# Kernel optimization log

Measured on AMD Instinct MI355X. Metric: run time of the kernel, lower is better.

## Reference

```python
import jax, jax.numpy as jnp
import numpy as np

N = 24000; E = 384000; NT = 3; IN = 128; HID = 32; ED = 64; NE = 5; FFN = 64; C = 16
HEADS = (8, 8, 1); ALPHA = 0.05; DAL = 2


def _lrelu(x, s):
    return jnp.where(x >= 0, x, s * x)


def _elu(x):
    return jnp.where(x > 0, x, jnp.expm1(x))


def _ln(x, g, b, eps=1e-5):
    m = x.mean(-1, keepdims=True)
    v = ((x - m) ** 2).mean(-1, keepdims=True)
    return (x - m) / jnp.sqrt(v + eps) * g + b


def _l2n(x, eps=1e-12):
    return x / jnp.maximum(jnp.linalg.norm(x, axis=1, keepdims=True), eps)


def _ta(h, src, dst, e_feat, edge_emb, W, We, al, ar, ae, bias, res_W, res_attn, act):
    # SimpleHGN-style heterogeneous graph attention layer (TALayer)
    Hh = al.shape[0]
    feat = (h @ W).reshape(N, Hh, HID)                       # [N,H,D]
    ee = (edge_emb[e_feat] @ We).reshape(E, Hh, ED)          # [E,H,ED]
    el = (feat * al).sum(-1)                                 # [N,H]
    er = (feat * ar).sum(-1)                                 # [N,H]
    lg = _lrelu(el[src] + er[dst] + (ee * ae).sum(-1), 0.2)  # [E,H]
    m = jax.ops.segment_max(lg, dst, num_segments=N)         # edge softmax over dst
    a = jnp.exp(lg - m[dst])
    a = a / jax.ops.segment_sum(a, dst, num_segments=N)[dst]
    if res_attn is not None:
        a = a * (1.0 - ALPHA) + res_attn * ALPHA             # residual attention carry-over
    rst = jax.ops.segment_sum(a[:, :, None] * feat[src], dst, num_segments=N)
    if res_W is not None:
        rst = rst + (h @ res_W).reshape(N, Hh, HID)
    rst = rst + bias
    if act:
        rst = _elu(rst)
    return rst, jax.lax.stop_gradient(a)


def forward(feats, fc_W, fc_b, ntype_emb, W_ntype,
            ta0_edge_emb, ta0_W, ta0_We, ta0_al, ta0_ar, ta0_ae, ta0_bias,
            ta1_edge_emb, ta1_W, ta1_We, ta1_al, ta1_ar, ta1_ae, ta1_bias, ta1_res_W,
            ta2_edge_emb, ta2_W, ta2_We, ta2_al, ta2_ar, ta2_ae, ta2_bias, ta2_res_W,
            da_ln1_g, da_ln1_b, da_Wq, da_bq, da_Wk, da_bk, da_Wv, da_bv, da_Wo, da_bo,
            da_ln2_g, da_ln2_b, da_W1, da_b1, da_W2, da_b2, final_W, logits_W,
            e_feat, node_type, src, dst):
    # per-node-type input projection + leaky_relu(0.01), concat over types -> [N,HID]
    h = _lrelu(jnp.einsum('tni,tio->tno', feats, fc_W) + fc_b[:, None, :], 0.01).reshape(N, HID)
    ntype_feat = (ntype_emb @ W_ntype)[node_type]            # [N,HID]
    h = h * ntype_feat
    h0, a0 = _ta(h, src, dst, e_feat, ta0_edge_emb, ta0_W, ta0_We, ta0_al, ta0_ar, ta0_ae, ta0_bias, None, None, True)
    h = h0.reshape(N, -1)
    h1, _ = _ta(h, src, dst, e_feat, ta1_edge_emb, ta1_W, ta1_We, ta1_al, ta1_ar, ta1_ae, ta1_bias, ta1_res_W, a0, True)
    h = h1.reshape(N, -1)
    hf, _ = _ta(h, src, dst, e_feat, ta2_edge_emb, ta2_W, ta2_We, ta2_al, ta2_ar, ta2_ae, ta2_bias, ta2_res_W, None, False)
    h_feat = hf.reshape(N, HID)
    # dim-wise transformer (DALayer stack): tokens = HID dims, channel = 1
    x = (h_feat * ntype_feat)[:, :, None]                    # [N,HID,1]
    for l in range(DAL):
        y = _ln(x, da_ln1_g[l], da_ln1_b[l])
        q = y @ da_Wq[l] + da_bq[l]
        k = y @ da_Wk[l] + da_bk[l]
        v = y @ da_Wv[l] + da_bv[l]
        att = jax.nn.softmax(jnp.einsum('nqd,nkd->nqk', q, k), axis=-1)  # scale=att_size**-0.5=1
        x = x + (jnp.einsum('nqk,nkd->nqd', att, v) @ da_Wo[l] + da_bo[l])
        y = _ln(x, da_ln2_g[l], da_ln2_b[l])
        x = x + (jax.nn.gelu(y @ da_W1[l] + da_b1[l], approximate=False) @ da_W2[l] + da_b2[l])
    h_dim = _l2n(x[:, :, 0])
    h_final = jnp.concatenate([_l2n(h_feat), h_dim], axis=1) @ final_W
    logits = jax.nn.relu(h_final) @ logits_W
    return logits / jnp.maximum(jnp.linalg.norm(logits, axis=1, keepdims=True), 1e-12)


def setup_inputs():
    key = jax.random.key(0)
    ks = iter(jax.random.split(key, 96))
    def rn(shape, s=0.1):
        return jax.random.normal(next(ks), shape, jnp.float32) * s
    inp = {}
    inp["feats"] = jax.random.normal(next(ks), (NT, N // NT, IN), jnp.float32)
    inp["e_feat"] = jax.random.randint(next(ks), (E,), 0, NE)
    inp["node_type"] = jax.random.randint(next(ks), (N,), 0, NT)
    inp["src"] = jax.random.randint(next(ks), (E,), 0, N)
    inp["dst"] = jax.random.randint(next(ks), (E,), 0, N)
    inp["fc_W"] = rn((NT, IN, HID)); inp["fc_b"] = rn((NT, HID))
    inp["ntype_emb"] = rn((NT, HID)); inp["W_ntype"] = rn((HID, HID))
    ins = (HID, HID * HEADS[0], HID * HEADS[1])
    for l in range(3):
        Hh = HEADS[l]; di = ins[l]; p = "ta%d_" % l
        inp[p + "edge_emb"] = rn((NE, ED))
        inp[p + "W"] = rn((di, Hh * HID))
        inp[p + "We"] = rn((ED, Hh * ED))
        inp[p + "al"] = rn((Hh, HID)); inp[p + "ar"] = rn((Hh, HID)); inp[p + "ae"] = rn((Hh, ED))
        inp[p + "bias"] = jnp.zeros((Hh, HID), jnp.float32)
        if l > 0:
            inp[p + "res_W"] = rn((di, Hh * HID))
    inp["da_ln1_g"] = jnp.ones((DAL, 1), jnp.float32); inp["da_ln1_b"] = jnp.zeros((DAL, 1), jnp.float32)
    inp["da_Wq"] = rn((DAL, 1, 1)); inp["da_bq"] = jnp.zeros((DAL, 1), jnp.float32)
    inp["da_Wk"] = rn((DAL, 1, 1)); inp["da_bk"] = jnp.zeros((DAL, 1), jnp.float32)
    inp["da_Wv"] = rn((DAL, 1, 1)); inp["da_bv"] = jnp.zeros((DAL, 1), jnp.float32)
    inp["da_Wo"] = rn((DAL, 1, 1)); inp["da_bo"] = jnp.zeros((DAL, 1), jnp.float32)
    inp["da_ln2_g"] = jnp.ones((DAL, 1), jnp.float32); inp["da_ln2_b"] = jnp.zeros((DAL, 1), jnp.float32)
    inp["da_W1"] = rn((DAL, 1, FFN)); inp["da_b1"] = jnp.zeros((DAL, FFN), jnp.float32)
    inp["da_W2"] = rn((DAL, FFN, 1)); inp["da_b2"] = jnp.zeros((DAL, 1), jnp.float32)
    inp["final_W"] = rn((2 * HID, HID))
    inp["logits_W"] = rn((HID, C))
    return inp


def reference(feats, fc_W, fc_b, ntype_emb, W_ntype,
              ta0_edge_emb, ta0_W, ta0_We, ta0_al, ta0_ar, ta0_ae, ta0_bias,
              ta1_edge_emb, ta1_W, ta1_We, ta1_al, ta1_ar, ta1_ae, ta1_bias, ta1_res_W,
              ta2_edge_emb, ta2_W, ta2_We, ta2_al, ta2_ar, ta2_ae, ta2_bias, ta2_res_W,
              da_ln1_g, da_ln1_b, da_Wq, da_bq, da_Wk, da_bk, da_Wv, da_bv, da_Wo, da_bo,
              da_ln2_g, da_ln2_b, da_W1, da_b1, da_W2, da_b2, final_W, logits_W,
              e_feat, node_type, src, dst):
    return forward(feats, fc_W, fc_b, ntype_emb, W_ntype,
                   ta0_edge_emb, ta0_W, ta0_We, ta0_al, ta0_ar, ta0_ae, ta0_bias,
                   ta1_edge_emb, ta1_W, ta1_We, ta1_al, ta1_ar, ta1_ae, ta1_bias, ta1_res_W,
                   ta2_edge_emb, ta2_W, ta2_We, ta2_al, ta2_ar, ta2_ae, ta2_bias, ta2_res_W,
                   da_ln1_g, da_ln1_b, da_Wq, da_bq, da_Wk, da_bk, da_Wv, da_bv, da_Wo, da_bo,
                   da_ln2_g, da_ln2_b, da_W1, da_b1, da_W2, da_b2, final_W, logits_W,
                   e_feat, node_type, src, dst)
```

## Files before the change

kernel.cpp:

```cpp
#include <hip/hip_runtime.h>
#include <math.h>

constexpr int kN = 24000;
constexpr int kE = 384000;
constexpr float kAlpha = 0.05f;

typedef unsigned int   u32;
typedef unsigned short u16;
typedef __attribute__((ext_vector_type(8))) short short8;
typedef __attribute__((ext_vector_type(4))) float float4v;

__device__ __forceinline__ float bf2f(u16 x) { return __uint_as_float(((u32)x) << 16); }
__device__ __forceinline__ u16 f2bf(float f) {
  u32 u = __float_as_uint(f);
  return (u16)((u + 0x7fffu + ((u >> 16) & 1u)) >> 16);
}

__global__ void __launch_bounds__(256) zero_ints_kernel(int* __restrict__ p, int n) {
  int i = blockIdx.x * 256 + threadIdx.x;
  if (i < n) p[i] = 0;
}

__global__ void __launch_bounds__(256) count_kernel(const int* __restrict__ dst,
                                                    int* __restrict__ counts) {
  int e = blockIdx.x * 256 + threadIdx.x;
  if (e < kE) atomicAdd(&counts[dst[e]], 1);
}

__global__ void __launch_bounds__(1024) scan_kernel(const int* __restrict__ counts,
                                                    int* __restrict__ row_start) {
  __shared__ int wsum[16];
  __shared__ int carry_s;
  int tid = threadIdx.x, lane = tid & 63, wid = tid >> 6;
  if (tid == 0) { carry_s = 0; row_start[0] = 0; }
  __syncthreads();
  for (int base = 0; base < kN; base += 1024) {
    int x = (base + tid < kN) ? counts[base + tid] : 0;
    #pragma unroll
    for (int off = 1; off < 64; off <<= 1) {
      int y = __shfl_up(x, off);
      if (lane >= off) x += y;
    }
    if (lane == 63) wsum[wid] = x;
    __syncthreads();
    if (tid < 16) {
      int wv = wsum[tid];
      #pragma unroll
      for (int off = 1; off < 16; off <<= 1) {
        int y = __shfl_up(wv, off);
        if (tid >= off) wv += y;
      }
      wsum[tid] = wv;
    }
    __syncthreads();
    int incl = x + carry_s + (wid > 0 ? wsum[wid - 1] : 0);
    if (base + tid < kN) row_start[base + tid + 1] = incl;
    __syncthreads();
    if (tid == 1023) carry_s = incl;
    __syncthreads();
  }
}

__global__ void __launch_bounds__(256) scatter_kernel(const int* __restrict__ dst,
                                                      const int* __restrict__ row_start,
                                                      int* __restrict__ cursor,
                                                      int* __restrict__ edge_ids) {
  int e = blockIdx.x * 256 + threadIdx.x;
  if (e < kE) {
    int n = dst[e];
    int pos = row_start[n] + atomicAdd(&cursor[n], 1);
    edge_ids[pos] = e;
  }
}

__global__ void __launch_bounds__(256) prepack_kernel(
    const float* __restrict__ W0, const float* __restrict__ al0, const float* __restrict__ ar0,
    const float* __restrict__ W1, const float* __restrict__ al1, const float* __restrict__ ar1,
    const float* __restrict__ rW1,
    const float* __restrict__ W2, const float* __restrict__ al2, const float* __restrict__ ar2,
    const float* __restrict__ rW2,
    u16* __restrict__ WT0, u16* __restrict__ WT1, u16* __restrict__ WT2,
    const float* __restrict__ ntype_emb, const float* __restrict__ W_ntype,
    const float* __restrict__ emb0, const float* __restrict__ We0, const float* __restrict__ ae0,
    const float* __restrict__ emb1, const float* __restrict__ We1, const float* __restrict__ ae1,
    const float* __restrict__ emb2, const float* __restrict__ We2, const float* __restrict__ ae2,
    const float* __restrict__ ln1_b, const float* __restrict__ Wv, const float* __restrict__ bv,
    const float* __restrict__ Wo, const float* __restrict__ bo,
    const float* __restrict__ ln2_b, const float* __restrict__ DW1, const float* __restrict__ Db1,
    const float* __restrict__ DW2, const float* __restrict__ Db2,
    float* __restrict__ ntf, float* __restrict__ eterm, float* __restrict__ dadelta) {
  __shared__ float wae[17][64];
  __shared__ float red[128];
  int tid = threadIdx.x;
  if (blockIdx.x < 744) {
    const int SZ0 = 320 * 32, SZ1 = 576 * 256;
    int gid = blockIdx.x * 256 + tid;
    float v = 0.f;
    if (gid < SZ0) {
      int n = gid / 32, k = gid % 32;
      if (n < 256) v = W0[k * 256 + n];
      else if (n < 264) { int h = n - 256; for (int d = 0; d < 32; ++d) v += W0[k * 256 + h * 32 + d] * al0[h * 32 + d]; }
      else if (n < 272) { int h = n - 264; for (int d = 0; d < 32; ++d) v += W0[k * 256 + h * 32 + d] * ar0[h * 32 + d]; }
      WT0[n * 32 + k] = f2bf(v);
    } else if (gid < SZ0 + SZ1) {
      int i = gid - SZ0;
      int n = i / 256, k = i % 256;
      if (n < 256) v = W1[k * 256 + n];
      else if (n < 264) { int h = n - 256; for (int d = 0; d < 32; ++d) v += W1[k * 256 + h * 32 + d] * al1[h * 32 + d]; }
      else if (n < 272) { int h = n - 264; for (int d = 0; d < 32; ++d) v += W1[k * 256 + h * 32 + d] * ar1[h * 32 + d]; }
      else if (n < 528) v = rW1[k * 256 + (n - 272)];
      WT1[n * 256 + k] = f2bf(v);
    } else {
      int i = gid - SZ0 - SZ1;
      int n = i / 256, k = i % 256;
      if (n < 32) v = W2[k * 32 + n];
      else if (n == 32) { for (int d = 0; d < 32; ++d) v += W2[k * 32 + d] * al2[d]; }
      else if (n == 33) { for (int d = 0; d < 32; ++d) v += W2[k * 32 + d] * ar2[d]; }
      else if (n < 66) v = rW2[k * 32 + (n - 34)];
      WT2[n * 256 + k] = f2bf(v);
    }
  } else {
    for (int idx = tid; idx < 17 * 64; idx += 256) {
      int hg = idx >> 6, k = idx & 63;
      const float* We; const float* ae; int Hh, h;
      if (hg < 8)       { We = We0; ae = ae0; Hh = 8; h = hg; }
      else if (hg < 16) { We = We1; ae = ae1; Hh = 8; h = hg - 8; }
      else              { We = We2; ae = ae2; Hh = 1; h = 0; }
      float s = 0.f;
      for (int d = 0; d < 64; ++d) s += We[(size_t)k * Hh * 64 + h * 64 + d] * ae[h * 64 + d];
      wae[hg][k] = s;
    }
    __syncthreads();
    for (int id = tid; id < 85; id += 256) {
      const float* emb; int Hh, t, h, hg, base;
      if (id < 40)      { emb = emb0; Hh = 8; t = id / 8;  h = id % 8; hg = h;      base = 0;  }
      else if (id < 80) { int i = id - 40; emb = emb1; Hh = 8; t = i / 8; h = i % 8; hg = 8 + h; base = 40; }
      else              { int i = id - 80; emb = emb2; Hh = 1; t = i;    h = 0;     hg = 16;    base = 80; }
      float s = 0.f;
      for (int k = 0; k < 64; ++k) s += emb[t * 64 + k] * wae[hg][k];
      eterm[base + t * Hh + h] = s;
    }
    for (int idx = tid; idx < 96; idx += 256) {
      int t = idx / 32, o = idx % 32;
      float s = 0.f;
      for (int k = 0; k < 32; ++k) s += ntype_emb[t * 32 + k] * W_ntype[k * 32 + o];
      ntf[idx] = s;
    }
    for (int i2 = tid; i2 < 128; i2 += 256) {
      int l = i2 >> 6, j = i2 & 63;
      float u = ln2_b[l] * DW1[l * 64 + j] + Db1[l * 64 + j];
      float g = 0.5f * u * (1.0f + erff(u * 0.7071067811865476f));
      red[i2] = g * DW2[l * 64 + j];
    }
    __syncthreads();
    if (tid == 0) {
      float delta = 0.f;
      for (int l = 0; l < 2; ++l) {
        float vs = ln1_b[l] * Wv[l] + bv[l];
        delta += vs * Wo[l] + bo[l] + Db2[l];
      }
      for (int i = 0; i < 128; ++i) delta += red[i];
      *dadelta = delta;
    }
  }
}

__global__ void __launch_bounds__(256) inproj_kernel(
    const float* __restrict__ feats, const float* __restrict__ fc_W,
    const float* __restrict__ fc_b, const float* __restrict__ ntf,
    const int* __restrict__ node_type, u16* __restrict__ hb) {
  int t = blockIdx.x * 256 + threadIdx.x;
  if (t >= kN * 32) return;
  int n = t >> 5, o = t & 31;
  int ty = n / 8000;
  const float* fr = &feats[(size_t)n * 128];
  const float* w  = &fc_W[(size_t)ty * 4096 + o];
  float s = fc_b[ty * 32 + o];
  #pragma unroll
  for (int k = 0; k < 128; k += 4) {
    float4 f = *(const float4*)&fr[k];
    s += f.x * w[(k + 0) * 32] + f.y * w[(k + 1) * 32]
       + f.z * w[(k + 2) * 32] + f.w * w[(k + 3) * 32];
  }
  s = (s < 0.f) ? 0.01f * s : s;
  hb[t] = f2bf(s * ntf[node_type[n] * 32 + o]);
}

template <int K>
__global__ void __launch_bounds__(256) mfma_gemm_kernel(
    const u16* __restrict__ A, const u16* __restrict__ WT,
    const float* __restrict__ bias,
    u16* __restrict__ featb, float* __restrict__ el, float* __restrict__ er,
    u16* __restrict__ resb, float* __restrict__ resf,
    int N1, int HH, int N2) {
  constexpr int RB = K * 2;
  constexpr int CPR = K / 8;
  __shared__ __align__(16) u16 As[64 * K];
  __shared__ __align__(16) u16 Bs[64 * K];
  const int tid = threadIdx.x;
  const int l = tid & 63;
  const int w = tid >> 6;
  const int wm = w >> 1, wn = w & 1;
  const int m0 = blockIdx.y * 64;
  const int n0 = blockIdx.x * 64;
  const int kslot = l >> 4;
  const int l15 = l & 15;

  #pragma unroll
  for (int c = tid; c < 64 * CPR; c += 256) {
    int row = c / CPR, ch = c - row * CPR;
    int off = (row * RB + ch * 16) ^ ((row & 7) << 4);
    uint4 va = *(const uint4*)(A + (size_t)(m0 + row) * K + ch * 8);
    *(uint4*)((char*)As + off) = va;
    uint4 vb = *(const uint4*)(WT + (size_t)(n0 + row) * K + ch * 8);
    *(uint4*)((char*)Bs + off) = vb;
  }
  __syncthreads();

  float4v acc[2][2];
  #pragma unroll
  for (int f = 0; f < 2; ++f)
    #pragma unroll
    for (int g = 0; g < 2; ++g) { acc[f][g][0]=0.f; acc[f][g][1]=0.f; acc[f][g][2]=0.f; acc[f][g][3]=0.f; }

  #pragma unroll
  for (int kc = 0; kc < K; kc += 32) {
    short8 af[2], bf[2];
    #pragma unroll
    for (int f = 0; f < 2; ++f) {
      int row = wm * 32 + f * 16 + l15;
      int off = (row * RB + kc * 2 + kslot * 16) ^ ((row & 7) << 4);
      af[f] = *(const short8*)((const char*)As + off);
    }
    #pragma unroll
    for (int g = 0; g < 2; ++g) {
      int n = wn * 32 + g * 16 + l15;
      int off = (n * RB + kc * 2 + kslot * 16) ^ ((n & 7) << 4);
      bf[g] = *(const short8*)((const char*)Bs + off);
    }
    #pragma unroll
    for (int f = 0; f < 2; ++f)
      #pragma unroll
      for (int g = 0; g < 2; ++g)
        acc[f][g] = __builtin_amdgcn_mfma_f32_16x16x32_bf16(af[f], bf[g], acc[f][g], 0, 0, 0);
  }

  const int rbase = kslot * 4;
  #pragma unroll
  for (int f = 0; f < 2; ++f) {
    #pragma unroll
    for (int g = 0; g < 2; ++g) {
      int gc = n0 + wn * 32 + g * 16 + l15;
      #pragma unroll
      for (int reg = 0; reg < 4; ++reg) {
        int gr = m0 + wm * 32 + f * 16 + rbase + reg;
        float v = acc[f][g][reg];
        if (gc < N1) {
          featb[(size_t)gr * N1 + gc] = f2bf(v);
        } else if (gc < N1 + HH) {
          el[(size_t)gr * HH + (gc - N1)] = v;
        } else if (gc < N1 + 2 * HH) {
          er[(size_t)gr * HH + (gc - N1 - HH)] = v;
        } else if (gc < N1 + 2 * HH + N2) {
          int c2 = gc - N1 - 2 * HH;
          float vv = v + bias[c2];
          if (resb) resb[(size_t)gr * N2 + c2] = f2bf(vv);
          else      resf[(size_t)gr * N2 + c2] = vv;
        }
      }
    }
  }
}

template <bool WRITE_A0, bool READ_A0, bool BIAS_INIT, bool ACT>
__global__ void __launch_bounds__(256) agg8w_kernel(
    const int* __restrict__ row_start, const int* __restrict__ edge_ids,
    const int* __restrict__ src, const int* __restrict__ ef,
    const float* __restrict__ el, const float* __restrict__ er,
    const float* __restrict__ eterm,
    const u16* __restrict__ featb,
    const float* __restrict__ bias,
    _Float16* __restrict__ a0h,
    const u16* __restrict__ accb,
    u16* __restrict__ outb) {
  int n = (blockIdx.x * 256 + threadIdx.x) >> 6;
  if (n >= kN) return;
  int l = threadIdx.x & 63;
  int h = l >> 3, s = l & 7;
  int s0 = row_start[n], s1 = row_start[n + 1];
  float ern = er[n * 8 + h];
  float et0 = eterm[0 * 8 + h], et1 = eterm[1 * 8 + h], et2 = eterm[2 * 8 + h];
  float et3 = eterm[3 * 8 + h], et4 = eterm[4 * 8 + h];
  float m = -1e30f, ssum = 0.f;
  for (int i = s0 + s; i < s1; i += 8) {
    int e = edge_ids[i];
    int efc = ef[e];
    float etv = (efc == 0) ? et0 : (efc == 1) ? et1 : (efc == 2) ? et2 : (efc == 3) ? et3 : et4;
    float lg = el[src[e] * 8 + h] + ern + etv;
    lg = (lg < 0.f) ? 0.2f * lg : lg;
    if (lg > m) { ssum = ssum * expf(m - lg) + 1.f; m = lg; }
    else        { ssum += expf(lg - m); }
  }
  #pragma unroll
  for (int mk = 1; mk <= 4; mk <<= 1) {
    float om = __shfl_xor(m, mk);
    float os = __shfl_xor(ssum, mk);
    float nm = fmaxf(m, om);
    ssum = ssum * expf(m - nm) + os * expf(om - nm);
    m = nm;
  }
  float inv = 1.f / ssum;
  const size_t rowoff = (size_t)n * 256 + h * 32 + s * 4;
  float4 acc;
  if (BIAS_INIT) {
    acc = *(const float4*)(bias + h * 32 + s * 4);
  } else {
    ushort4 rv = *(const ushort4*)(accb + rowoff);
    acc = make_float4(bf2f(rv.x), bf2f(rv.y), bf2f(rv.z), bf2f(rv.w));
  }
  int i = s0;
  for (; i + 8 <= s1; i += 8) {
    int e = edge_ids[i + s];
    int sek = src[e];
    int efc = ef[e];
    float etv = (efc == 0) ? et0 : (efc == 1) ? et1 : (efc == 2) ? et2 : (efc == 3) ? et3 : et4;
    float lg = el[sek * 8 + h] + ern + etv;
    lg = (lg < 0.f) ? 0.2f * lg : lg;
    float am = expf(lg - m) * inv;
    if (WRITE_A0) a0h[(size_t)e * 8 + h] = (_Float16)am;
    if (READ_A0)  am = am * (1.f - kAlpha) + (float)a0h[(size_t)e * 8 + h] * kAlpha;
    #pragma unroll
    for (int j = 0; j < 8; ++j) {
      float aj = __shfl(am, (h << 3) + j);
      int sej = __shfl(sek, j);
      ushort4 fv = *(const ushort4*)(featb + (size_t)sej * 256 + h * 32 + s * 4);
      acc.x = fmaf(aj, bf2f(fv.x), acc.x);
      acc.y = fmaf(aj, bf2f(fv.y), acc.y);
      acc.z = fmaf(aj, bf2f(fv.z), acc.z);
      acc.w = fmaf(aj, bf2f(fv.w), acc.w);
    }
  }
  if (i < s1) {
    int cnt = s1 - i;
    float am = 0.f; int sek = 0;
    if (s < cnt) {
      int e = edge_ids[i + s];
      sek = src[e];
      int efc = ef[e];
      float etv = (efc == 0) ? et0 : (efc == 1) ? et1 : (efc == 2) ? et2 : (efc == 3) ? et3 : et4;
      float lg = el[sek * 8 + h] + ern + etv;
      lg = (lg < 0.f) ? 0.2f * lg : lg;
      am = expf(lg - m) * inv;
      if (WRITE_A0) a0h[(size_t)e * 8 + h] = (_Float16)am;
      if (READ_A0)  am = am * (1.f - kAlpha) + (float)a0h[(size_t)e * 8 + h] * kAlpha;
    }
    for (int j = 0; j < cnt; ++j) {
      float aj = __shfl(am, (h << 3) + j);
      int sej = __shfl(sek, j);
      ushort4 fv = *(const ushort4*)(featb + (size_t)sej * 256 + h * 32 + s * 4);
      acc.x = fmaf(aj, bf2f(fv.x), acc.x);
      acc.y = fmaf(aj, bf2f(fv.y), acc.y);
      acc.z = fmaf(aj, bf2f(fv.z), acc.z);
      acc.w = fmaf(aj, bf2f(fv.w), acc.w);
    }
  }
  if (ACT) {
    acc.x = (acc.x > 0.f) ? acc.x : expm1f(acc.x);
    acc.y = (acc.y > 0.f) ? acc.y : expm1f(acc.y);
    acc.z = (acc.z > 0.f) ? acc.z : expm1f(acc.z);
    acc.w = (acc.w > 0.f) ? acc.w : expm1f(acc.w);
  }
  ushort4 pw;
  pw.x = f2bf(acc.x); pw.y = f2bf(acc.y); pw.z = f2bf(acc.z); pw.w = f2bf(acc.w);
  *(ushort4*)(outb + rowoff) = pw;
}

__global__ void __launch_bounds__(256) aggw1_final_kernel(
    const int* __restrict__ row_start, const int* __restrict__ edge_ids,
    const int* __restrict__ src, const int* __restrict__ ef,
    const float* __restrict__ el, const float* __restrict__ er,
    const float* __restrict__ eterm,
    const u16* __restrict__ featb,
    const float* __restrict__ S2,
    const float* __restrict__ ntf, const int* __restrict__ node_type,
    const float* __restrict__ dadelta,
    const float* __restrict__ finalW, const float* __restrict__ logitsW,
    float* __restrict__ out) {
  __shared__ float fWs[2048];
  __shared__ float lWs[512];
  __shared__ float abuf[8][32];
  __shared__ float bbuf[8][32];
  __shared__ float sbuf[8][32];
  const int tid = threadIdx.x;
  for (int i = tid; i < 2048; i += 256) fWs[i] = finalW[i];
  for (int i = tid; i < 512; i += 256) lWs[i] = logitsW[i];
  const int slot = tid >> 5;
  const int g = tid & 31;
  const int gb = tid & 32;
  const int n = blockIdx.x * 8 + slot;
  const int s0 = row_start[n], s1 = row_start[n + 1];
  float ern = er[n];
  float et0 = eterm[0], et1 = eterm[1], et2 = eterm[2], et3 = eterm[3], et4 = eterm[4];
  float m = -1e30f, ssum = 0.f;
  for (int i = s0 + g; i < s1; i += 32) {
    int e = edge_ids[i];
    int efc = ef[e];
    float etv = (efc == 0) ? et0 : (efc == 1) ? et1 : (efc == 2) ? et2 : (efc == 3) ? et3 : et4;
    float lg = el[src[e]] + ern + etv;
    lg = (lg < 0.f) ? 0.2f * lg : lg;
    if (lg > m) { ssum = ssum * expf(m - lg) + 1.f; m = lg; }
    else        { ssum += expf(lg - m); }
  }
  #pragma unroll
  for (int mk = 1; mk <= 16; mk <<= 1) {
    float om = __shfl_xor(m, mk);
    float os = __shfl_xor(ssum, mk);
    float nm = fmaxf(m, om);
    ssum = ssum * expf(m - nm) + os * expf(om - nm);
    m = nm;
  }
  float inv = 1.f / ssum;
  float acc = S2[(size_t)n * 32 + g];
  int i = s0;
  for (; i + 32 <= s1; i += 32) {
    int e = edge_ids[i + g];
    int sek = src[e];
    int efc = ef[e];
    float etv = (efc == 0) ? et0 : (efc == 1) ? et1 : (efc == 2) ? et2 : (efc == 3) ? et3 : et4;
    float lg = el[sek] + ern + etv;
    lg = (lg < 0.f) ? 0.2f * lg : lg;
    float am = expf(lg - m) * inv;
    #pragma unroll
    for (int j = 0; j < 32; ++j) {
      float aj = __shfl(am, gb + j);
      int sej = __shfl(sek, gb + j);
      acc = fmaf(aj, bf2f(featb[(size_t)sej * 32 + g]), acc);
    }
  }
  if (i < s1) {
    int cnt = s1 - i;
    float am = 0.f; int sek = 0;
    if (g < cnt) {
      int e = edge_ids[i + g];
      sek = src[e];
      int efc = ef[e];
      float etv = (efc == 0) ? et0 : (efc == 1) ? et1 : (efc == 2) ? et2 : (efc == 3) ? et3 : et4;
      float lg = el[sek] + ern + etv;
      lg = (lg < 0.f) ? 0.2f * lg : lg;
      am = expf(lg - m) * inv;
    }
    for (int j = 0; j < cnt; ++j) {
      float aj = __shfl(am, gb + j);
      int sej = __shfl(sek, gb + j);
      acc = fmaf(aj, bf2f(featb[(size_t)sej * 32 + g]), acc);
    }
  }
  float delta = dadelta[0];
  float ntv = ntf[node_type[n] * 32 + g];
  float av = acc;
  float bv = acc * ntv + delta;
  float na = av * av, nb = bv * bv;
  #pragma unroll
  for (int mk = 1; mk <= 16; mk <<= 1) {
    na += __shfl_xor(na, mk);
    nb += __shfl_xor(nb, mk);
  }
  float inva = 1.f / fmaxf(sqrtf(na), 1e-12f);
  float invb = 1.f / fmaxf(sqrtf(nb), 1e-12f);
  __syncthreads();
  abuf[slot][g] = av * inva;
  bbuf[slot][g] = bv * invb;
  __syncthreads();
  float s = 0.f;
  #pragma unroll
  for (int d = 0; d < 32; ++d)
    s += abuf[slot][d] * fWs[d * 32 + g] + bbuf[slot][d] * fWs[(32 + d) * 32 + g];
  s = fmaxf(s, 0.f);
  sbuf[slot][g] = s;
  __syncthreads();
  if (g < 16) {
    float lg = 0.f;
    #pragma unroll
    for (int o = 0; o < 32; ++o) lg += sbuf[slot][o] * lWs[o * 16 + g];
    float nl = lg * lg;
    #pragma unroll
    for (int mk = 1; mk <= 8; mk <<= 1) nl += __shfl_xor(nl, mk);
    float invl = 1.f / fmaxf(sqrtf(nl), 1e-12f);
    out[(size_t)n * 16 + g] = lg * invl;
  }
}

extern "C" void kernel_launch(void* const* d_in, const int* in_sizes, int n_in,
                              void* d_out, int out_size, void* d_ws, size_t ws_size,
                              hipStream_t stream) {
  const float* feats     = (const float*)d_in[0];
  const int*   e_feat    = (const int*)d_in[1];
  const int*   node_type = (const int*)d_in[2];
  const int*   src       = (const int*)d_in[3];
  const int*   dst       = (const int*)d_in[4];
  const float* fc_W      = (const float*)d_in[5];
  const float* fc_b      = (const float*)d_in[6];
  const float* ntype_emb = (const float*)d_in[7];
  const float* W_ntype   = (const float*)d_in[8];
  const float* ta_edge_emb[3] = {(const float*)d_in[9],  (const float*)d_in[16], (const float*)d_in[24]};
  const float* ta_W[3]        = {(const float*)d_in[10], (const float*)d_in[17], (const float*)d_in[25]};
  const float* ta_We[3]       = {(const float*)d_in[11], (const float*)d_in[18], (const float*)d_in[26]};
  const float* ta_al[3]       = {(const float*)d_in[12], (const float*)d_in[19], (const float*)d_in[27]};
  const float* ta_ar[3]       = {(const float*)d_in[13], (const float*)d_in[20], (const float*)d_in[28]};
  const float* ta_ae[3]       = {(const float*)d_in[14], (const float*)d_in[21], (const float*)d_in[29]};
  const float* ta_bias[3]     = {(const float*)d_in[15], (const float*)d_in[22], (const float*)d_in[30]};
  const float* ta1_res_W = (const float*)d_in[23];
  const float* ta2_res_W = (const float*)d_in[31];
  const float* da_ln1_b  = (const float*)d_in[33];
  const float* da_Wv     = (const float*)d_in[38];
  const float* da_bv     = (const float*)d_in[39];
  const float* da_Wo     = (const float*)d_in[40];
  const float* da_bo     = (const float*)d_in[41];
  const float* da_ln2_b  = (const float*)d_in[43];
  const float* da_W1     = (const float*)d_in[44];
  const float* da_b1     = (const float*)d_in[45];
  const float* da_W2     = (const float*)d_in[46];
  const float* da_b2     = (const float*)d_in[47];
  const float* final_W   = (const float*)d_in[48];
  const float* logits_W  = (const float*)d_in[49];
  float* out = (float*)d_out;

  char* base = (char*)d_ws;
  int* iws       = (int*)base;
  int* counts    = iws;
  int* cursor    = iws + kN;
  int* row_start = iws + 2 * kN;
  int* edge_ids  = iws + 2 * kN + kN + 1;
  char* p = base + (size_t)456004 * 4;
  float* ntf = (float*)p;                     p += 512;
  float* etm = (float*)p;                     p += 512;
  float* dad = (float*)p;                     p += 64;
  float* el  = (float*)p;                     p += (size_t)kN * 8 * 4;
  float* er  = (float*)p;                     p += (size_t)kN * 8 * 4;
  float* S2  = (float*)p;                     p += (size_t)kN * 32 * 4;
  u16*   Hb  = (u16*)p;                       p += (size_t)kN * 32 * 2;
  _Float16* a0h = (_Float16*)p;               p += (size_t)kE * 8 * 2;
  u16* featb = (u16*)p;                       p += (size_t)kN * 256 * 2;
  u16* Rb0   = (u16*)p;                       p += (size_t)kN * 256 * 2;
  u16* Rpr   = (u16*)p;                       p += (size_t)kN * 256 * 2;
  u16* WT0   = (u16*)p;                       p += (size_t)320 * 32 * 2;
  u16* WT1   = (u16*)p;                       p += (size_t)576 * 256 * 2;
  u16* WT2   = (u16*)p;                       p += (size_t)128 * 256 * 2;

  zero_ints_kernel<<<(2 * kN + 255) / 256, 256, 0, stream>>>(counts, 2 * kN);
  count_kernel<<<kE / 256, 256, 0, stream>>>(dst, counts);
  scan_kernel<<<1, 1024, 0, stream>>>(counts, row_start);
  scatter_kernel<<<kE / 256, 256, 0, stream>>>(dst, row_start, cursor, edge_ids);

  prepack_kernel<<<745, 256, 0, stream>>>(
      ta_W[0], ta_al[0], ta_ar[0],
      ta_W[1], ta_al[1], ta_ar[1], ta1_res_W,
      ta_W[2], ta_al[2], ta_ar[2], ta2_res_W,
      WT0, WT1, WT2,
      ntype_emb, W_ntype,
      ta_edge_emb[0], ta_We[0], ta_ae[0],
      ta_edge_emb[1], ta_We[1], ta_ae[1],
      ta_edge_emb[2], ta_We[2], ta_ae[2],
      da_ln1_b, da_Wv, da_bv, da_Wo, da_bo,
      da_ln2_b, da_W1, da_b1, da_W2, da_b2,
      ntf, etm, dad);

  inproj_kernel<<<(kN * 32) / 256, 256, 0, stream>>>(feats, fc_W, fc_b, ntf, node_type, Hb);

  mfma_gemm_kernel<32><<<dim3(5, kN / 64), 256, 0, stream>>>(
      Hb, WT0, nullptr, featb, el, er, nullptr, nullptr, 256, 8, 0);
  agg8w_kernel<true, false, true, true><<<kN / 4, 256, 0, stream>>>(
      row_start, edge_ids, src, e_feat, el, er, etm, featb, ta_bias[0], a0h, nullptr, Rb0);

  mfma_gemm_kernel<256><<<dim3(9, kN / 64), 256, 0, stream>>>(
      Rb0, WT1, ta_bias[1], featb, el, er, Rpr, nullptr, 256, 8, 256);
  agg8w_kernel<false, true, false, true><<<kN / 4, 256, 0, stream>>>(
      row_start, edge_ids, src, e_feat, el, er, etm + 40, featb, nullptr, a0h, Rpr, Rpr);

  mfma_gemm_kernel<256><<<dim3(2, kN / 64), 256, 0, stream>>>(
      Rpr, WT2, ta_bias[2], featb, el, er, nullptr, S2, 32, 1, 32);
  aggw1_final_kernel<<<kN / 8, 256, 0, stream>>>(
      row_start, edge_ids, src, e_feat, el, er, etm + 80, featb, S2,
      ntf, node_type, dad, final_W, logits_W, out);
}
```

Before: 487.2 us.

## Aggregate layer-0 on 32-dim inputs before projection, then block-diagonal GEMM

Layer 0 now computes only el/er with the GEMM, aggregates the 32-wide input features per head (gather of 64 bytes per edge instead of 512), and then applies each head's 32x32 projection in a new block-diagonal MFMA kernel with fused bias and ELU. The generic GEMM is also restructured so each block keeps its A tile in shared memory and loops over all column tiles, avoiding repeated A loads across grid columns. The cost is an extra kernel launch and an intermediate per-head buffer of aggregated features. Rounding also changes because aggregation now runs before projection.

```diff
diff --git a/kernel.cpp b/kernel.cpp
--- a/kernel.cpp
+++ b/kernel.cpp
@@ -93,15 +93,18 @@
   __shared__ float red[128];
   int tid = threadIdx.x;
   if (blockIdx.x < 744) {
-    const int SZ0 = 320 * 32, SZ1 = 576 * 256;
+    const int SZ0 = 10240, SZ1 = 576 * 256;
     int gid = blockIdx.x * 256 + tid;
     float v = 0.f;
-    if (gid < SZ0) {
+    if (gid < 2048) {
       int n = gid / 32, k = gid % 32;
-      if (n < 256) v = W0[k * 256 + n];
-      else if (n < 264) { int h = n - 256; for (int d = 0; d < 32; ++d) v += W0[k * 256 + h * 32 + d] * al0[h * 32 + d]; }
-      else if (n < 272) { int h = n - 264; for (int d = 0; d < 32; ++d) v += W0[k * 256 + h * 32 + d] * ar0[h * 32 + d]; }
+      if (n < 8)       { for (int d = 0; d < 32; ++d) v += W0[k * 256 + n * 32 + d] * al0[n * 32 + d]; }
+      else if (n < 16) { int h = n - 8; for (int d = 0; d < 32; ++d) v += W0[k * 256 + h * 32 + d] * ar0[h * 32 + d]; }
       WT0[n * 32 + k] = f2bf(v);
+    } else if (gid < SZ0) {
+      int i = gid - 2048;
+      int h = i >> 10, rem = i & 1023, d = rem >> 5, k = rem & 31;
+      WT0[2048 + i] = f2bf(W0[k * 256 + h * 32 + d]);
     } else if (gid < SZ0 + SZ1) {
       int i = gid - SZ0;
       int n = i / 256, k = i % 256;
@@ -192,7 +195,7 @@
     const float* __restrict__ bias,
     u16* __restrict__ featb, float* __restrict__ el, float* __restrict__ er,
     u16* __restrict__ resb, float* __restrict__ resf,
-    int N1, int HH, int N2) {
+    int NT, int N1, int HH, int N2) {
   constexpr int RB = K * 2;
   constexpr int CPR = K / 8;
   __shared__ __align__(16) u16 As[64 * K];
@@ -201,8 +204,7 @@
   const int l = tid & 63;
   const int w = tid >> 6;
   const int wm = w >> 1, wn = w & 1;
-  const int m0 = blockIdx.y * 64;
-  const int n0 = blockIdx.x * 64;
+  const int m0 = blockIdx.x * 64;
   const int kslot = l >> 4;
   const int l15 = l & 15;
 
@@ -210,77 +212,226 @@
   for (int c = tid; c < 64 * CPR; c += 256) {
     int row = c / CPR, ch = c - row * CPR;
     int off = (row * RB + ch * 16) ^ ((row & 7) << 4);
-    uint4 va = *(const uint4*)(A + (size_t)(m0 + row) * K + ch * 8);
-    *(uint4*)((char*)As + off) = va;
-    uint4 vb = *(const uint4*)(WT + (size_t)(n0 + row) * K + ch * 8);
-    *(uint4*)((char*)Bs + off) = vb;
-  }
-  __syncthreads();
-
-  float4v acc[2][2];
-  #pragma unroll
-  for (int f = 0; f < 2; ++f)
-    #pragma unroll
-    for (int g = 0; g < 2; ++g) { acc[f][g][0]=0.f; acc[f][g][1]=0.f; acc[f][g][2]=0.f; acc[f][g][3]=0.f; }
-
-  #pragma unroll
-  for (int kc = 0; kc < K; kc += 32) {
-    short8 af[2], bf[2];
-    #pragma unroll
-    for (int f = 0; f < 2; ++f) {
-      int row = wm * 32 + f * 16 + l15;
-      int off = (row * RB + kc * 2 + kslot * 16) ^ ((row & 7) << 4);
-      af[f] = *(const short8*)((const char*)As + off);
-    }
-    #pragma unroll
-    for (int g = 0; g < 2; ++g) {
-      int n = wn * 32 + g * 16 + l15;
-      int off = (n * RB + kc * 2 + kslot * 16) ^ ((n & 7) << 4);
-      bf[g] = *(const short8*)((const char*)Bs + off);
-    }
+    *(uint4*)((char*)As + off) = *(const uint4*)(A + (size_t)(m0 + row) * K + ch * 8);
+  }
+
+  for (int ct = 0; ct < NT; ++ct) {
+    __syncthreads();
+    #pragma unroll
+    for (int c = tid; c < 64 * CPR; c += 256) {
+      int row = c / CPR, ch = c - row * CPR;
+      int off = (row * RB + ch * 16) ^ ((row & 7) << 4);
+      *(uint4*)((char*)Bs + off) = *(const uint4*)(WT + (size_t)(ct * 64 + row) * K + ch * 8);
+    }
+    __syncthreads();
+
+    float4v acc[2][2];
     #pragma unroll
     for (int f = 0; f < 2; ++f)
       #pragma unroll
-      for (int g = 0; g < 2; ++g)
-        acc[f][g] = __builtin_amdgcn_mfma_f32_16x16x32_bf16(af[f], bf[g], acc[f][g], 0, 0, 0);
-  }
-
-  const int rbase = kslot * 4;
-  #pragma unroll
-  for (int f = 0; f < 2; ++f) {
-    #pragma unroll
-    for (int g = 0; g < 2; ++g) {
-      int gc = n0 + wn * 32 + g * 16 + l15;
+      for (int g = 0; g < 2; ++g) { acc[f][g][0]=0.f; acc[f][g][1]=0.f; acc[f][g][2]=0.f; acc[f][g][3]=0.f; }
+
+    #pragma unroll
+    for (int kc = 0; kc < K; kc += 32) {
+      short8 af[2], bf[2];
       #pragma unroll
-      for (int reg = 0; reg < 4; ++reg) {
-        int gr = m0 + wm * 32 + f * 16 + rbase + reg;
-        float v = acc[f][g][reg];
-        if (gc < N1) {
-          featb[(size_t)gr * N1 + gc] = f2bf(v);
-        } else if (gc < N1 + HH) {
-          el[(size_t)gr * HH + (gc - N1)] = v;
-        } else if (gc < N1 + 2 * HH) {
-          er[(size_t)gr * HH + (gc - N1 - HH)] = v;
-        } else if (gc < N1 + 2 * HH + N2) {
-          int c2 = gc - N1 - 2 * HH;
-          float vv = v + bias[c2];
-          if (resb) resb[(size_t)gr * N2 + c2] = f2bf(vv);
-          else      resf[(size_t)gr * N2 + c2] = vv;
+      for (int f = 0; f < 2; ++f) {
+        int row = wm * 32 + f * 16 + l15;
+        int off = (row * RB + kc * 2 + kslot * 16) ^ ((row & 7) << 4);
+        af[f] = *(const short8*)((const char*)As + off);
+      }
+      #pragma unroll
+      for (int g = 0; g < 2; ++g) {
+        int n = wn * 32 + g * 16 + l15;
+        int off = (n * RB + kc * 2 + kslot * 16) ^ ((n & 7) << 4);
+        bf[g] = *(const short8*)((const char*)Bs + off);
+      }
+      #pragma unroll
+      for (int f = 0; f < 2; ++f)
+        #pragma unroll
+        for (int g = 0; g < 2; ++g)
+          acc[f][g] = __builtin_amdgcn_mfma_f32_16x16x32_bf16(af[f], bf[g], acc[f][g], 0, 0, 0);
+    }
+
+    const int rbase = kslot * 4;
+    #pragma unroll
+    for (int f = 0; f < 2; ++f) {
+      #pragma unroll
+      for (int g = 0; g < 2; ++g) {
+        int gc = ct * 64 + wn * 32 + g * 16 + l15;
+        #pragma unroll
+        for (int reg = 0; reg < 4; ++reg) {
+          int gr = m0 + wm * 32 + f * 16 + rbase + reg;
+          float v = acc[f][g][reg];
+          if (gc < N1) {
+            featb[(size_t)gr * N1 + gc] = f2bf(v);
+          } else if (gc < N1 + HH) {
+            el[(size_t)gr * HH + (gc - N1)] = v;
+          } else if (gc < N1 + 2 * HH) {
+            er[(size_t)gr * HH + (gc - N1 - HH)] = v;
+          } else if (gc < N1 + 2 * HH + N2) {
+            int c2 = gc - N1 - 2 * HH;
+            float vv = v + bias[c2];
+            if (resb) resb[(size_t)gr * N2 + c2] = f2bf(vv);
+            else      resf[(size_t)gr * N2 + c2] = vv;
+          }
         }
       }
     }
   }
 }
 
-template <bool WRITE_A0, bool READ_A0, bool BIAS_INIT, bool ACT>
+__global__ void __launch_bounds__(256) agg8h_kernel(
+    const int* __restrict__ row_start, const int* __restrict__ edge_ids,
+    const int* __restrict__ src, const int* __restrict__ ef,
+    const float* __restrict__ el, const float* __restrict__ er,
+    const float* __restrict__ eterm,
+    const u16* __restrict__ Hb,
+    _Float16* __restrict__ a0h,
+    u16* __restrict__ Gb) {
+  int n = (blockIdx.x * 256 + threadIdx.x) >> 6;
+  if (n >= kN) return;
+  int l = threadIdx.x & 63;
+  int h = l >> 3, s = l & 7;
+  int s0 = row_start[n], s1 = row_start[n + 1];
+  float ern = er[n * 8 + h];
+  float et0 = eterm[0 * 8 + h], et1 = eterm[1 * 8 + h], et2 = eterm[2 * 8 + h];
+  float et3 = eterm[3 * 8 + h], et4 = eterm[4 * 8 + h];
+  float m = -1e30f, ssum = 0.f;
+  for (int i = s0 + s; i < s1; i += 8) {
+    int e = edge_ids[i];
+    int efc = ef[e];
+    float etv = (efc == 0) ? et0 : (efc == 1) ? et1 : (efc == 2) ? et2 : (efc == 3) ? et3 : et4;
+    float lg = el[src[e] * 8 + h] + ern + etv;
+    lg = (lg < 0.f) ? 0.2f * lg : lg;
+    if (lg > m) { ssum = ssum * expf(m - lg) + 1.f; m = lg; }
+    else        { ssum += expf(lg - m); }
+  }
+  #pragma unroll
+  for (int mk = 1; mk <= 4; mk <<= 1) {
+    float om = __shfl_xor(m, mk);
+    float os = __shfl_xor(ssum, mk);
+    float nm = fmaxf(m, om);
+    ssum = ssum * expf(m - nm) + os * expf(om - nm);
+    m = nm;
+  }
+  float inv = 1.f / ssum;
+  float4 acc = make_float4(0.f, 0.f, 0.f, 0.f);
+  int i = s0;
+  for (; i + 8 <= s1; i += 8) {
+    int e = edge_ids[i + s];
+    int sek = src[e];
+    int efc = ef[e];
+    float etv = (efc == 0) ? et0 : (efc == 1) ? et1 : (efc == 2) ? et2 : (efc == 3) ? et3 : et4;
+    float lg = el[sek * 8 + h] + ern + etv;
+    lg = (lg < 0.f) ? 0.2f * lg : lg;
+    float am = expf(lg - m) * inv;
+    a0h[(size_t)e * 8 + h] = (_Float16)am;
+    #pragma unroll
+    for (int j = 0; j < 8; ++j) {
+      float aj = __shfl(am, (h << 3) + j);
+      int sej = __shfl(sek, j);
+      ushort4 fv = *(const ushort4*)(Hb + (size_t)sej * 32 + s * 4);
+      acc.x = fmaf(aj, bf2f(fv.x), acc.x);
+      acc.y = fmaf(aj, bf2f(fv.y), acc.y);
+      acc.z = fmaf(aj, bf2f(fv.z), acc.z);
+      acc.w = fmaf(aj, bf2f(fv.w), acc.w);
+    }
+  }
+  if (i < s1) {
+    int cnt = s1 - i;
+    float am = 0.f; int sek = 0;
+    if (s < cnt) {
+      int e = edge_ids[i + s];
+      sek = src[e];
+      int efc = ef[e];
+      float etv = (efc == 0) ? et0 : (efc == 1) ? et1 : (efc == 2) ? et2 : (efc == 3) ? et3 : et4;
+      float lg = el[sek * 8 + h] + ern + etv;
+      lg = (lg < 0.f) ? 0.2f * lg : lg;
+      am = expf(lg - m) * inv;
+      a0h[(size_t)e * 8 + h] = (_Float16)am;
+    }
+    for (int j = 0; j < cnt; ++j) {
+      float aj = __shfl(am, (h << 3) + j);
+      int sej = __shfl(sek, j);
+      ushort4 fv = *(const ushort4*)(Hb + (size_t)sej * 32 + s * 4);
+      acc.x = fmaf(aj, bf2f(fv.x), acc.x);
+      acc.y = fmaf(aj, bf2f(fv.y), acc.y);
+      acc.z = fmaf(aj, bf2f(fv.z), acc.z);
+      acc.w = fmaf(aj, bf2f(fv.w), acc.w);
+    }
+  }
+  ushort4 pw;
+  pw.x = f2bf(acc.x); pw.y = f2bf(acc.y); pw.z = f2bf(acc.z); pw.w = f2bf(acc.w);
+  *(ushort4*)(Gb + (size_t)n * 256 + h * 32 + s * 4) = pw;
+}
+
+__global__ void __launch_bounds__(256) bd_gemm_kernel(
+    const u16* __restrict__ Gb,
+    const u16* __restrict__ WbdT,
+    const float* __restrict__ bias,
+    u16* __restrict__ outb) {
+  __shared__ __align__(16) u16 As[64 * 256];
+  __shared__ __align__(16) u16 Bs[8 * 32 * 32];
+  const int tid = threadIdx.x;
+  const int l = tid & 63;
+  const int w = tid >> 6;
+  const int m0 = blockIdx.x * 64;
+  const int kslot = l >> 4, l15 = l & 15;
+  for (int c = tid; c < 64 * 32; c += 256) {
+    int row = c >> 5, ch = c & 31;
+    int off = (row * 512 + ch * 16) ^ ((row & 7) << 4);
+    *(uint4*)((char*)As + off) = *(const uint4*)(Gb + (size_t)(m0 + row) * 256 + ch * 8);
+  }
+  for (int c = tid; c < 256 * 4; c += 256) {
+    int r = c >> 2, ch = c & 3;
+    int off = (r * 64 + ch * 16) ^ ((r & 7) << 4);
+    *(uint4*)((char*)Bs + off) = *(const uint4*)(WbdT + (size_t)r * 32 + ch * 8);
+  }
+  __syncthreads();
+  #pragma unroll
+  for (int hh = 0; hh < 2; ++hh) {
+    int h = w * 2 + hh;
+    short8 af[4];
+    #pragma unroll
+    for (int f = 0; f < 4; ++f) {
+      int row = f * 16 + l15;
+      int off = (row * 512 + h * 64 + kslot * 16) ^ ((row & 7) << 4);
+      af[f] = *(const short8*)((const char*)As + off);
+    }
+    short8 bf[2];
+    #pragma unroll
+    for (int g = 0; g < 2; ++g) {
+      int r = h * 32 + g * 16 + l15;
+      int off = (r * 64 + kslot * 16) ^ ((r & 7) << 4);
+      bf[g] = *(const short8*)((const char*)Bs + off);
+    }
+    #pragma unroll
+    for (int f = 0; f < 4; ++f) {
+      #pragma unroll
+      for (int g = 0; g < 2; ++g) {
+        float4v acc = {0.f, 0.f, 0.f, 0.f};
+        acc = __builtin_amdgcn_mfma_f32_16x16x32_bf16(af[f], bf[g], acc, 0, 0, 0);
+        #pragma unroll
+        for (int reg = 0; reg < 4; ++reg) {
+          int gr = m0 + f * 16 + kslot * 4 + reg;
+          int gc = h * 32 + g * 16 + l15;
+          float v = acc[reg] + bias[gc];
+          v = (v > 0.f) ? v : expm1f(v);
+          outb[(size_t)gr * 256 + gc] = f2bf(v);
+        }
+      }
+    }
+  }
+}
+
 __global__ void __launch_bounds__(256) agg8w_kernel(
     const int* __restrict__ row_start, const int* __restrict__ edge_ids,
     const int* __restrict__ src, const int* __restrict__ ef,
     const float* __restrict__ el, const float* __restrict__ er,
     const float* __restrict__ eterm,
     const u16* __restrict__ featb,
-    const float* __restrict__ bias,
-    _Float16* __restrict__ a0h,
+    const _Float16* __restrict__ a0h,
     const u16* __restrict__ accb,
     u16* __restrict__ outb) {
   int n = (blockIdx.x * 256 + threadIdx.x) >> 6;
@@ -311,13 +462,8 @@
   }
   float inv = 1.f / ssum;
   const size_t rowoff = (size_t)n * 256 + h * 32 + s * 4;
-  float4 acc;
-  if (BIAS_INIT) {
-    acc = *(const float4*)(bias + h * 32 + s * 4);
-  } else {
-    ushort4 rv = *(const ushort4*)(accb + rowoff);
-    acc = make_float4(bf2f(rv.x), bf2f(rv.y), bf2f(rv.z), bf2f(rv.w));
-  }
+  ushort4 rv = *(const ushort4*)(accb + rowoff);
+  float4 acc = make_float4(bf2f(rv.x), bf2f(rv.y), bf2f(rv.z), bf2f(rv.w));
   int i = s0;
   for (; i + 8 <= s1; i += 8) {
     int e = edge_ids[i + s];
@@ -327,8 +473,7 @@
     float lg = el[sek * 8 + h] + ern + etv;
     lg = (lg < 0.f) ? 0.2f * lg : lg;
     float am = expf(lg - m) * inv;
-    if (WRITE_A0) a0h[(size_t)e * 8 + h] = (_Float16)am;
-    if (READ_A0)  am = am * (1.f - kAlpha) + (float)a0h[(size_t)e * 8 + h] * kAlpha;
+    am = am * (1.f - kAlpha) + (float)a0h[(size_t)e * 8 + h] * kAlpha;
     #pragma unroll
     for (int j = 0; j < 8; ++j) {
       float aj = __shfl(am, (h << 3) + j);
@@ -351,8 +496,7 @@
       float lg = el[sek * 8 + h] + ern + etv;
       lg = (lg < 0.f) ? 0.2f * lg : lg;
       am = expf(lg - m) * inv;
-      if (WRITE_A0) a0h[(size_t)e * 8 + h] = (_Float16)am;
-      if (READ_A0)  am = am * (1.f - kAlpha) + (float)a0h[(size_t)e * 8 + h] * kAlpha;
+      am = am * (1.f - kAlpha) + (float)a0h[(size_t)e * 8 + h] * kAlpha;
     }
     for (int j = 0; j < cnt; ++j) {
       float aj = __shfl(am, (h << 3) + j);
@@ -364,12 +508,10 @@
       acc.w = fmaf(aj, bf2f(fv.w), acc.w);
     }
   }
-  if (ACT) {
-    acc.x = (acc.x > 0.f) ? acc.x : expm1f(acc.x);
-    acc.y = (acc.y > 0.f) ? acc.y : expm1f(acc.y);
-    acc.z = (acc.z > 0.f) ? acc.z : expm1f(acc.z);
-    acc.w = (acc.w > 0.f) ? acc.w : expm1f(acc.w);
-  }
+  acc.x = (acc.x > 0.f) ? acc.x : expm1f(acc.x);
+  acc.y = (acc.y > 0.f) ? acc.y : expm1f(acc.y);
+  acc.z = (acc.z > 0.f) ? acc.z : expm1f(acc.z);
+  acc.w = (acc.w > 0.f) ? acc.w : expm1f(acc.w);
   ushort4 pw;
   pw.x = f2bf(acc.x); pw.y = f2bf(acc.y); pw.z = f2bf(acc.z); pw.w = f2bf(acc.w);
   *(ushort4*)(outb + rowoff) = pw;
@@ -546,6 +688,8 @@
   u16* WT0   = (u16*)p;                       p += (size_t)320 * 32 * 2;
   u16* WT1   = (u16*)p;                       p += (size_t)576 * 256 * 2;
   u16* WT2   = (u16*)p;                       p += (size_t)128 * 256 * 2;
+  u16* WT0el = WT0;
+  u16* Wbd0T = WT0 + 2048;
 
   zero_ints_kernel<<<(2 * kN + 255) / 256, 256, 0, stream>>>(counts, 2 * kN);
   count_kernel<<<kE / 256, 256, 0, stream>>>(dst, counts);
@@ -567,18 +711,19 @@
 
   inproj_kernel<<<(kN * 32) / 256, 256, 0, stream>>>(feats, fc_W, fc_b, ntf, node_type, Hb);
 
-  mfma_gemm_kernel<32><<<dim3(5, kN / 64), 256, 0, stream>>>(
-      Hb, WT0, nullptr, featb, el, er, nullptr, nullptr, 256, 8, 0);
-  agg8w_kernel<true, false, true, true><<<kN / 4, 256, 0, stream>>>(
-      row_start, edge_ids, src, e_feat, el, er, etm, featb, ta_bias[0], a0h, nullptr, Rb0);
-
-  mfma_gemm_kernel<256><<<dim3(9, kN / 64), 256, 0, stream>>>(
-      Rb0, WT1, ta_bias[1], featb, el, er, Rpr, nullptr, 256, 8, 256);
-  agg8w_kernel<false, true, false, true><<<kN / 4, 256, 0, stream>>>(
-      row_start, edge_ids, src, e_feat, el, er, etm + 40, featb, nullptr, a0h, Rpr, Rpr);
-
-  mfma_gemm_kernel<256><<<dim3(2, kN / 64), 256, 0, stream>>>(
-      Rpr, WT2, ta_bias[2], featb, el, er, nullptr, S2, 32, 1, 32);
+  mfma_gemm_kernel<32><<<kN / 64, 256, 0, stream>>>(
+      Hb, WT0el, nullptr, nullptr, el, er, nullptr, nullptr, 1, 0, 8, 0);
+  agg8h_kernel<<<kN / 4, 256, 0, stream>>>(
+      row_start, edge_ids, src, e_feat, el, er, etm, Hb, a0h, featb);
+  bd_gemm_kernel<<<kN / 64, 256, 0, stream>>>(featb, Wbd0T, ta_bias[0], Rb0);
+
+  mfma_gemm_kernel<256><<<kN / 64, 256, 0, stream>>>(
+      Rb0, WT1, ta_bias[1], featb, el, er, Rpr, nullptr, 9, 256, 8, 256);
+  agg8w_kernel<<<kN / 4, 256, 0, stream>>>(
+      row_start, edge_ids, src, e_feat, el, er, etm + 40, featb, a0h, Rpr, Rpr);
+
+  mfma_gemm_kernel<256><<<kN / 64, 256, 0, stream>>>(
+      Rpr, WT2, ta_bias[2], featb, el, er, nullptr, S2, 2, 32, 1, 32);
   aggw1_final_kernel<<<kN / 8, 256, 0, stream>>>(
       row_start, edge_ids, src, e_feat, el, er, etm + 80, featb, S2,
       ntf, node_type, dad, final_W, logits_W, out);
```

Result: no change. 490.0 us (+0.6%).
